# Kernel optimization log

Measured on AMD Instinct MI355X. Metric: run time of the kernel, lower is better.

The kernel has to match this reference:

```python
import jax, jax.numpy as jnp
import numpy as np

# ---- config constants (match init_kwargs / MjModel camera params) ----
PAD_RES = (255, 255)          # padded sensor resolution (Mx, My), odd
RES = (160, 160)              # eye resolution (target_width, target_height)
APERTURE = 0.1                # aperture as fraction of sensor half-size
WAVELENGTHS = (6.1e-07, 5.3e-07, 4.7e-07)  # RGB wavelengths [m]
SENSOR_SIZE = (2e-3, 2e-3)    # (sx, sy) from MjModel.cam_sensorsize [m]


def setup_inputs() -> dict:
    key = jax.random.key(0)
    k1, k2 = jax.random.split(key)
    image = jax.random.uniform(k1, (PAD_RES[0], PAD_RES[1], 3), dtype=jnp.float32)
    depth = jax.random.uniform(k2, (PAD_RES[0], PAD_RES[1]), dtype=jnp.float32)
    return {"image": image, "depth": depth}


def _optics_consts():
    """Precompute the grids of MjCambrianOptics._reset_psf."""
    Mx, My = PAD_RES
    sx, sy = SENSOR_SIZE
    dx, dy = sx / Mx, sy / My
    Lx, Ly = dx * Mx, dy * My
    x1 = jnp.linspace(-Lx / 2.0, Lx / 2.0, Mx, dtype=jnp.float32)
    y1 = jnp.linspace(-Ly / 2.0, Ly / 2.0, My, dtype=jnp.float32)
    X1, Y1 = jnp.meshgrid(x1, y1, indexing='ij')
    fx = jnp.linspace(-1.0 / (2.0 * dx), 1.0 / (2.0 * dx), Mx, dtype=jnp.float32)
    fy = jnp.linspace(-1.0 / (2.0 * dx), 1.0 / (2.0 * dx), My, dtype=jnp.float32)  # dx for both, faithful to source
    FX, FY = jnp.meshgrid(fx, fy, indexing='ij')
    aperture_radius = min(Lx / 2, Ly / 2) * APERTURE + 1e-07
    A = (jnp.sqrt(X1**2 + Y1**2) / aperture_radius <= 1.0).astype(jnp.float32)
    wl = jnp.asarray(WAVELENGTHS, dtype=jnp.float32)[:, None, None]  # (3,1,1)
    X1_Y1 = X1**2 + Y1**2                                           # (Mx,My)
    H_valid = (jnp.sqrt(FX**2 + FY**2) < 1.0 / wl).astype(jnp.float32)  # (3,Mx,My)
    arg = 1.0 - (wl * FX) ** 2 - (wl * FY) ** 2
    # Source computes sqrt(arg) (NaN where arg<0) then nan_to_num after exp;
    # H_valid is exactly 0 where arg<=0, so clamping arg to 0 yields the same H.
    FX_FY = jnp.sqrt(jnp.maximum(arg, 0.0))                         # (3,Mx,My)
    k = (1j * 2.0 * jnp.pi / wl).astype(jnp.complex64)              # (3,1,1)
    return A, X1_Y1, H_valid, FX_FY, k


def _depth_invariant_psf(mean_depth):
    A, X1_Y1, H_valid, FX_FY, k = _optics_consts()
    # spherical wave from point source at mean_depth, masked by aperture
    u1 = jnp.exp(k * jnp.sqrt(X1_Y1 + mean_depth**2))   # (3,Mx,My) complex64
    u2 = u1 * A
    # angular-spectrum transfer function
    H = H_valid * jnp.exp(k * mean_depth * FX_FY)
    u3 = jnp.fft.ifft2(jnp.fft.fft2(H) * jnp.fft.fft2(u2))
    psf = u3 * u3                                        # complex square, faithful to torch.square
    psf = psf / (jnp.sum(psf) + 1e-07)                   # complex normalization, faithful
    return jnp.real(psf)                                 # (3,Mx,My) float32


def reference(image, depth):
    psf = _depth_invariant_psf(jnp.mean(depth))          # (3,Mx,My)
    img = jnp.transpose(image, (2, 0, 1))[None]          # (1,3,H,W)
    kern = psf[:, None].astype(img.dtype)                # (3,1,Mx,My)
    out = jax.lax.conv_general_dilated(
        img, kern, window_strides=(1, 1), padding='SAME',
        feature_group_count=3, dimension_numbers=('NCHW', 'OIHW', 'NCHW'))
    out = jnp.transpose(out[0], (1, 2, 0))               # (H,W,3)
    width, height = out.shape[0], out.shape[1]
    target_width, target_height = RES
    top = (height - target_height) // 2
    left = (width - target_width) // 2
    out = out[top:top + target_height, left:left + target_width]
    return jnp.clip(out, 0.0, 1.0)
```

## Files before the change

kernel.cpp:

```cpp
#include <hip/hip_runtime.h>
#include <hip/hip_bf16.h>
#include <math.h>


constexpr int M   = 255;
constexpr int NP  = M * M;
constexpr int RESO = 160;

constexpr int IMG_ROWS = 416, IMG_COLS = 448;
constexpr int IMG_CH   = IMG_ROWS * IMG_COLS;
constexpr int IMG_SIDE = 3 * IMG_CH;
constexpr int P4_DI   = 304 * 8;
constexpr int P4_CH   = 256 * P4_DI;
constexpr int P4_SIDE = 3 * P4_CH;

typedef __attribute__((ext_vector_type(8))) short short8;
typedef __attribute__((ext_vector_type(4))) float f32x4;

__device__ __forceinline__ unsigned short f2bf(float f) {
    unsigned int u = __float_as_uint(f);
    unsigned int r = (u + 0x7fffu + ((u >> 16) & 1u)) >> 16;
    return (unsigned short)r;
}
__device__ __forceinline__ float bf2f(unsigned short h) {
    return __uint_as_float(((unsigned int)h) << 16);
}

constexpr int MAXN = 1100;
struct PWForest {
    int kind[MAXN];
    int off[MAXN], len[MAXN];
    int li[MAXN], ri[MAXN];
    int lvl[MAXN];
    int nNode, nLeaf, maxLvl;
    int roots[16], nRoots;
};
constexpr int pwf_build(PWForest& T, int o, int n) {
    if (n <= 128) {
        int id = T.nNode++;
        T.kind[id] = 0; T.off[id] = o; T.len[id] = n;
        T.lvl[id] = 0; T.nLeaf++;
        return id;
    }
    int n2 = (n / 2) - ((n / 2) % 8);
    int a = pwf_build(T, o, n2);
    int b = pwf_build(T, o + n2, n - n2);
    int id = T.nNode++;
    T.kind[id] = 1; T.li[id] = a; T.ri[id] = b;
    int l = (T.lvl[a] > T.lvl[b] ? T.lvl[a] : T.lvl[b]) + 1;
    T.lvl[id] = l; if (l > T.maxLvl) T.maxLvl = l;
    return id;
}
constexpr PWForest pwf_make() {
    PWForest T{};
    int pos = 1, rem = NP - 1;
    while (rem > 0) {
        int c = rem > 8192 ? 8192 : rem;
        T.roots[T.nRoots++] = pwf_build(T, pos, c);
        pos += c; rem -= c;
    }
    return T;
}
constexpr PWForest PW = pwf_make();
static_assert(PW.nNode <= MAXN, "forest overflow");
static_assert(PW.nRoots == 8, "chunk count");

__global__ void k_mleaf(const float* __restrict__ depth, float* __restrict__ val) {
    int id = blockIdx.x * 256 + threadIdx.x;
    if (id >= PW.nNode || PW.kind[id] != 0) return;
    const float* a = depth + PW.off[id];
    int n = PW.len[id];
    float r0 = a[0], r1 = a[1], r2 = a[2], r3 = a[3];
    float r4 = a[4], r5 = a[5], r6 = a[6], r7 = a[7];
    int lim = n - (n % 8);
    int i = 8;
    for (; i < lim; i += 8) {
        r0 += a[i + 0]; r1 += a[i + 1]; r2 += a[i + 2]; r3 += a[i + 3];
        r4 += a[i + 4]; r5 += a[i + 5]; r6 += a[i + 6]; r7 += a[i + 7];
    }
    float res = ((r0 + r1) + (r2 + r3)) + ((r4 + r5) + (r6 + r7));
    for (; i < n; ++i) res += a[i];
    val[id] = res;
}

__global__ void k_mtree(const float* __restrict__ depth, float* __restrict__ val,
                        float* __restrict__ meanp) {
    int tid = threadIdx.x;
    for (int l = 1; l <= PW.maxLvl; ++l) {
        for (int id = tid; id < PW.nNode; id += 256)
            if (PW.kind[id] == 1 && PW.lvl[id] == l)
                val[id] = val[PW.li[id]] + val[PW.ri[id]];
        __syncthreads();
    }
    if (tid == 0) {
        float io1 = depth[0];
        for (int r = 0; r < PW.nRoots; ++r)
            io1 = io1 + val[PW.roots[r]];
        meanp[0] = io1 / 65025.0f;
    }
}

__global__ void k_prep(const float* __restrict__ img, unsigned short* __restrict__ IMG2,
                       float2* __restrict__ W,
                       float2* __restrict__ U2, float2* __restrict__ Hb,
                       const float* __restrict__ meanp,
                       double xstart, double xstep, double xstop,
                       double fstart, double fstep, double fstop,
                       float ap_f) {
#pragma clang fp contract(off)
    int idx = blockIdx.x * 256 + threadIdx.x;
    if (idx < 3 * NP) {
        int c = idx / NP, ij = idx % NP, i = ij / M, j = ij % M;
        const float wls[3] = {6.1e-07f, 5.3e-07f, 4.7e-07f};
        float wl = wls[c];
        float ki = ((float)6.283185307179586) / wl;
        float d  = meanp[0];
        float d2 = d * d;

        float x  = (i == 254) ? (float)xstop : (float)((double)i * xstep + xstart);
        float y  = (j == 254) ? (float)xstop : (float)((double)j * xstep + xstart);
        float fx = (i == 254) ? (float)fstop : (float)((double)i * fstep + fstart);
        float fy = (j == 254) ? (float)fstop : (float)((double)j * fstep + fstart);

        float xx = x * x, yy = y * y;
        float X1Y1 = xx + yy;

        float s  = sqrtf(X1Y1 + d2);
        float th = ki * s;
        float A  = (sqrtf(X1Y1) / ap_f <= 1.0f) ? 1.0f : 0.0f;
        float2 u2v;
        if (A != 0.0f) u2v = make_float2((float)cos((double)th), (float)sin((double)th));
        else           u2v = make_float2(0.0f, 0.0f);

        float a = wl * fx, b = wl * fy;
        float arg = (1.0f - a * a) - b * b;
        float FXY = sqrtf(fmaxf(arg, 0.0f));
        float Hv  = (sqrtf(fx * fx + fy * fy) < (1.0f / wl)) ? 1.0f : 0.0f;
        float kd  = ki * d;
        float ph  = kd * FXY;
        float cph = (float)cos((double)ph), sph = (float)sin((double)ph);
        float2 hv = make_float2(Hv * cph, Hv * sph);

        U2[idx] = u2v;
        Hb[idx] = hv;
        return;
    }
    if (idx < 4 * NP) {
        int e = idx - 3 * NP;
        int n = e / M, k = e % M;
        int m = (n * k) % M;
        double ang = -2.0 * 3.14159265358979323846 * (double)m / 255.0;
        W[e] = make_float2((float)cos(ang), (float)sin(ang));
        return;
    }
    int e = idx - 4 * NP;
    if (e >= IMG_SIDE) return;
    int ch = e / IMG_CH, rem = e % IMG_CH;
    int prow = rem / IMG_COLS, pcol = rem % IMG_COLS;
    int a = prow - 80, b = pcol - 80;
    float v = 0.0f;
    if (a >= 0 && a < M && b >= 0 && b < M) v = img[(a * M + b) * 3 + ch];
    unsigned short hi = f2bf(v);
    unsigned short lo = f2bf(v - bf2f(hi));
    IMG2[e] = hi;
    IMG2[IMG_SIDE + e] = lo;
}

#define CG_LOAD(KT, VA0, WB0, VA1, WB1) { \
    int k0_ = (KT) * 16; \
    { int idx_ = threadIdx.x; \
      int r_ = idx_ >> 4, cc_ = idx_ & 15; \
      int gi_ = i0 + r_, gk_ = k0_ + cc_; \
      VA0 = (gi_ < M && gk_ < M) ? Ab[gi_ * M + gk_] : make_float2(0.f, 0.f); \
      if (conjA) VA0.y = -VA0.y; \
      int r2_ = idx_ >> 5, c2_ = idx_ & 31; \
      int gk2_ = k0_ + r2_, gj_ = j0 + c2_; \
      WB0 = make_float2(0.f, 0.f); \
      if (gk2_ < M && gj_ < M) { \
          WB0 = Bb[gk2_ * M + gj_]; \
          if (B2b) { float2 z_ = B2b[gk2_ * M + gj_]; \
              WB0 = make_float2(WB0.x * z_.x - WB0.y * z_.y, WB0.x * z_.y + WB0.y * z_.x); } \
      } \
      if (conjB) WB0.y = -WB0.y; } \
    { int idx_ = threadIdx.x + 256; \
      int r_ = idx_ >> 4, cc_ = idx_ & 15; \
      int gi_ = i0 + r_, gk_ = k0_ + cc_; \
      VA1 = (gi_ < M && gk_ < M) ? Ab[gi_ * M + gk_] : make_float2(0.f, 0.f); \
      if (conjA) VA1.y = -VA1.y; \
      int r2_ = idx_ >> 5, c2_ = idx_ & 31; \
      int gk2_ = k0_ + r2_, gj_ = j0 + c2_; \
      WB1 = make_float2(0.f, 0.f); \
      if (gk2_ < M && gj_ < M) { \
          WB1 = Bb[gk2_ * M + gj_]; \
          if (B2b) { float2 z_ = B2b[gk2_ * M + gj_]; \
              WB1 = make_float2(WB1.x * z_.x - WB1.y * z_.y, WB1.x * z_.y + WB1.y * z_.x); } \
      } \
      if (conjB) WB1.y = -WB1.y; } }

__global__ __launch_bounds__(256)
void k_cgemm(const float2* __restrict__ A, int aBatch,
             const float2* __restrict__ B, const float2* __restrict__ B2,
             int bBatch, float2* __restrict__ C,
             int conjA, int conjB, float scale) {
    __shared__ float2 As[32][17];
    __shared__ float2 Bs[16][33];
    int c = blockIdx.z;
    int tx = threadIdx.x & 15, ty = threadIdx.x >> 4;
    int i0 = blockIdx.y * 32, j0 = blockIdx.x * 32;
    const float2* Ab = A + (size_t)c * aBatch;
    const float2* Bb = B + (size_t)c * bBatch;
    const float2* B2b = B2 ? (B2 + (size_t)c * bBatch) : nullptr;
    float2 a00 = {0,0}, a01 = {0,0}, a10 = {0,0}, a11 = {0,0};

    int wr0 = threadIdx.x >> 4,  wc0 = threadIdx.x & 15;
    int wr0b = threadIdx.x >> 5, wc0b = threadIdx.x & 31;
    int wr1 = (threadIdx.x + 256) >> 4,  wc1 = (threadIdx.x + 256) & 15;
    int wr1b = (threadIdx.x + 256) >> 5, wc1b = (threadIdx.x + 256) & 31;

    float2 vA0, wB0, vA1, wB1;
    float2 nA0, nB0, nA1, nB1;
    CG_LOAD(0, vA0, wB0, vA1, wB1)

    for (int kt = 0; kt < 16; ++kt) {
        As[wr0][wc0]   = vA0;  Bs[wr0b][wc0b] = wB0;
        As[wr1][wc1]   = vA1;  Bs[wr1b][wc1b] = wB1;
        if (kt < 15) { CG_LOAD(kt + 1, nA0, nB0, nA1, nB1) }
        __syncthreads();
#pragma unroll
        for (int kk = 0; kk < 16; ++kk) {
            float2 p = As[ty][kk], q = As[ty + 16][kk];
            float2 u = Bs[kk][tx], v = Bs[kk][tx + 16];
            a00.x += p.x * u.x - p.y * u.y;  a00.y += p.x * u.y + p.y * u.x;
            a01.x += p.x * v.x - p.y * v.y;  a01.y += p.x * v.y + p.y * v.x;
            a10.x += q.x * u.x - q.y * u.y;  a10.y += q.x * u.y + q.y * u.x;
            a11.x += q.x * v.x - q.y * v.y;  a11.y += q.x * v.y + q.y * v.x;
        }
        __syncthreads();
        vA0 = nA0; wB0 = nB0; vA1 = nA1; wB1 = nB1;
    }
    float2* Cb = C + (size_t)c * NP;
    int gi0 = i0 + ty, gi1 = i0 + ty + 16;
    int gj0 = j0 + tx, gj1 = j0 + tx + 16;
    if (gi0 < M && gj0 < M) Cb[gi0 * M + gj0] = make_float2(a00.x * scale, a00.y * scale);
    if (gi0 < M && gj1 < M) Cb[gi0 * M + gj1] = make_float2(a01.x * scale, a01.y * scale);
    if (gi1 < M && gj0 < M) Cb[gi1 * M + gj0] = make_float2(a10.x * scale, a10.y * scale);
    if (gi1 < M && gj1 < M) Cb[gi1 * M + gj1] = make_float2(a11.x * scale, a11.y * scale);
}

__global__ void k_sred(const float2* __restrict__ U3, double2* __restrict__ spart) {
    __shared__ double sx[256], sy[256];
    int t = threadIdx.x;
    double ax = 0.0, ay = 0.0;
    for (int i = blockIdx.x * 256 + t; i < 3 * NP; i += 64 * 256) {
        double zx = (double)U3[i].x, zy = (double)U3[i].y;
        ax += zx * zx - zy * zy;
        ay += 2.0 * zx * zy;
    }
    sx[t] = ax; sy[t] = ay;
    __syncthreads();
    for (int w = 128; w > 0; w >>= 1) {
        if (t < w) { sx[t] += sx[t + w]; sy[t] += sy[t + w]; }
        __syncthreads();
    }
    if (t == 0) spart[blockIdx.x] = make_double2(sx[0], sy[0]);
}

__global__ void k_sfin(const double2* __restrict__ spart, double* __restrict__ sfin) {
    if (threadIdx.x != 0 || blockIdx.x != 0) return;
    double rx = 0.0, ry = 0.0;
    for (int i = 0; i < 64; ++i) { rx += spart[i].x; ry += spart[i].y; }
    double dsx = rx + 1e-7, dsy = ry;
    sfin[0] = dsx;
    sfin[1] = dsy;
    sfin[2] = 1.0 / (dsx * dsx + dsy * dsy);
}

__global__ void k_p4(const float2* __restrict__ U3, const double* __restrict__ sfin,
                     unsigned short* __restrict__ P4) {
    int idx = blockIdx.x * 256 + threadIdx.x;
    if (idx >= P4_SIDE) return;
    double dsx = sfin[0], dsy = sfin[1], inv = sfin[2];
    int ch = idx / P4_CH, rem = idx % P4_CH;
    int di = rem / P4_DI, rem2 = rem % P4_DI;
    int u = rem2 / 8, t = rem2 % 8;
    int p = u - 16 + t;
    float v = 0.0f;
    if (di < M && p >= 0 && p < M) {
        float2 zf = U3[(ch * M + di) * M + p];
        double zx = (double)zf.x, zy = (double)zf.y;
        double zr = zx * zx - zy * zy;
        double zi = 2.0 * zx * zy;
        v = (float)((zr * dsx + zi * dsy) * inv);
    }
    unsigned short hi = f2bf(v);
    unsigned short lo = f2bf(v - bf2f(hi));
    P4[idx] = hi;
    P4[P4_SIDE + idx] = lo;
}

constexpr int LDS_STRIDE = 312;

#define SB __builtin_amdgcn_sched_barrier(0);

#define REP9(OP) OP(0) OP(1) OP(2) OP(3) OP(4) OP(5) OP(6) OP(7) OP(8)

#define DECLA(i) short8 Ah_##i, Al_##i;
#define DECLB(i) short8 Bh_##i, Bl_##i;

#define LDA(i) Ah_##i = *(const short8*)(prH + 256 * i); \
               Al_##i = *(const short8*)(prL + 256 * i);
#define LDB(i) Bh_##i = *(const short8*)(prH + 256 * i); \
               Bl_##i = *(const short8*)(prL + 256 * i);
#define LOADA(dl) { const unsigned short* prH = pHc + (size_t)(d0 + (dl)) * P4_DI + aoff; \
                    const unsigned short* prL = pLc + (size_t)(d0 + (dl)) * P4_DI + aoff; \
                    REP9(LDA) }
#define LOADB(dl) { const unsigned short* prH = pHc + (size_t)(d0 + (dl)) * P4_DI + aoff; \
                    const unsigned short* prL = pLc + (size_t)(d0 + (dl)) * P4_DI + aoff; \
                    REP9(LDB) }

#define CMA(i) { \
    short8 bh0 = *(const short8*)&ldsI[0][rrow][32 * i + 8 * q]; \
    short8 bl0 = *(const short8*)&ldsI[1][rrow][32 * i + 8 * q]; \
    short8 bh1 = *(const short8*)&ldsI[0][rrow][32 * i + 8 * q + 16]; \
    short8 bl1 = *(const short8*)&ldsI[1][rrow][32 * i + 8 * q + 16]; \
    aHH0 = __builtin_amdgcn_mfma_f32_16x16x32_bf16(Ah_##i, bh0, aHH0, 0, 0, 0); \
    aHL0 = __builtin_amdgcn_mfma_f32_16x16x32_bf16(Ah_##i, bl0, aHL0, 0, 0, 0); \
    aLH0 = __builtin_amdgcn_mfma_f32_16x16x32_bf16(Al_##i, bh0, aLH0, 0, 0, 0); \
    aHH1 = __builtin_amdgcn_mfma_f32_16x16x32_bf16(Ah_##i, bh1, aHH1, 0, 0, 0); \
    aHL1 = __builtin_amdgcn_mfma_f32_16x16x32_bf16(Ah_##i, bl1, aHL1, 0, 0, 0); \
    aLH1 = __builtin_amdgcn_mfma_f32_16x16x32_bf16(Al_##i, bh1, aLH1, 0, 0, 0); }
#define CMB(i) { \
    short8 bh0 = *(const short8*)&ldsI[0][rrow][32 * i + 8 * q]; \
    short8 bl0 = *(const short8*)&ldsI[1][rrow][32 * i + 8 * q]; \
    short8 bh1 = *(const short8*)&ldsI[0][rrow][32 * i + 8 * q + 16]; \
    short8 bl1 = *(const short8*)&ldsI[1][rrow][32 * i + 8 * q + 16]; \
    aHH0 = __builtin_amdgcn_mfma_f32_16x16x32_bf16(Bh_##i, bh0, aHH0, 0, 0, 0); \
    aHL0 = __builtin_amdgcn_mfma_f32_16x16x32_bf16(Bh_##i, bl0, aHL0, 0, 0, 0); \
    aLH0 = __builtin_amdgcn_mfma_f32_16x16x32_bf16(Bl_##i, bh0, aLH0, 0, 0, 0); \
    aHH1 = __builtin_amdgcn_mfma_f32_16x16x32_bf16(Bh_##i, bh1, aHH1, 0, 0, 0); \
    aHL1 = __builtin_amdgcn_mfma_f32_16x16x32_bf16(Bh_##i, bl1, aHL1, 0, 0, 0); \
    aLH1 = __builtin_amdgcn_mfma_f32_16x16x32_bf16(Bl_##i, bh1, aLH1, 0, 0, 0); }
#define COMPA(dl) { int rrow = ln + (dl); REP9(CMA) }
#define COMPB(dl) { int rrow = ln + (dl); REP9(CMB) }

__global__ __launch_bounds__(256, 2)
void k_conv(const unsigned short* __restrict__ IMG2,
            const unsigned short* __restrict__ P4,
            float* __restrict__ PART) {
    __shared__ __align__(16) unsigned short ldsI[2][31][LDS_STRIDE];

    int tid  = threadIdx.x;
    int w    = tid >> 6;
    int lane = tid & 63;
    int ln   = lane & 15;
    int q    = lane >> 4;
    int j0 = blockIdx.x * 32;
    int i0 = blockIdx.y * 16;
    int bz = blockIdx.z;
    int ch = bz >> 4, chunk = bz & 15;
    int d0 = chunk << 4;

    const unsigned short* imgH = IMG2 + ch * IMG_CH;
    const unsigned short* imgL = imgH + IMG_SIDE;
    const unsigned short* pHc  = P4 + ch * P4_CH;
    const unsigned short* pLc  = pHc + P4_SIDE;

    int su0  = 16 + 8 * q - ln;
    int aoff = su0 * 8;

    f32x4 aHH0 = {0.f,0.f,0.f,0.f}, aHL0 = {0.f,0.f,0.f,0.f}, aLH0 = {0.f,0.f,0.f,0.f};
    f32x4 aHH1 = {0.f,0.f,0.f,0.f}, aHL1 = {0.f,0.f,0.f,0.f}, aLH1 = {0.f,0.f,0.f,0.f};

    REP9(DECLA)
    REP9(DECLB)

    int dbase = 4 * w;
    LOADA(dbase + 0)

    int row0 = i0 + d0;
    for (int idx = tid; idx < 2 * 31 * 38; idx += 256) {
        int plane = idx / (31 * 38);
        int rem = idx - plane * (31 * 38);
        int r = rem / 38, c = rem - r * 38;
        const unsigned short* src =
            (plane ? imgL : imgH) + (size_t)(row0 + r) * IMG_COLS + j0 + c * 8;
        *(short8*)&ldsI[plane][r][c * 8] = *(const short8*)src;
    }
    __syncthreads();

    LOADB(dbase + 1)
    SB
    COMPA(dbase + 0)
    SB
    LOADA(dbase + 2)
    SB
    COMPB(dbase + 1)
    SB
    LOADB(dbase + 3)
    SB
    COMPA(dbase + 2)
    SB
    COMPB(dbase + 3)

    f32x4 tot0, tot1;
#pragma unroll
    for (int r = 0; r < 4; ++r) {
        tot0[r] = aHH0[r] + aHL0[r] + aLH0[r];
        tot1[r] = aHH1[r] + aHL1[r] + aLH1[r];
    }

    __syncthreads();
    float* red = (float*)&ldsI[0][0][0];
    if (w) {
#pragma unroll
        for (int r = 0; r < 4; ++r) {
            red[((w - 1) * 64 + lane) * 8 + r]     = tot0[r];
            red[((w - 1) * 64 + lane) * 8 + 4 + r] = tot1[r];
        }
    }
    __syncthreads();
    if (w == 0) {
#pragma unroll
        for (int wv = 0; wv < 3; ++wv)
#pragma unroll
            for (int r = 0; r < 4; ++r) {
                tot0[r] += red[(wv * 64 + lane) * 8 + r];
                tot1[r] += red[(wv * 64 + lane) * 8 + 4 + r];
            }
        float* op = PART + (size_t)bz * (RESO * RESO) + (i0 + ln) * RESO + j0 + 4 * q;
        float4 o0; o0.x = tot0[0]; o0.y = tot0[1]; o0.z = tot0[2]; o0.w = tot0[3];
        float4 o1; o1.x = tot1[0]; o1.y = tot1[1]; o1.z = tot1[2]; o1.w = tot1[3];
        *(float4*)op = o0;
        *(float4*)(op + 16) = o1;
    }
}

__global__ void k_out(const float* __restrict__ PART, float* __restrict__ out) {
    int idx = blockIdx.x * 256 + threadIdx.x;
    if (idx >= 3 * RESO * RESO) return;
    int c = idx / (RESO * RESO), ij = idx % (RESO * RESO);
    float s = 0.0f;
    for (int kz = 0; kz < 16; ++kz)
        s += PART[(size_t)(c * 16 + kz) * (RESO * RESO) + ij];
    s = fminf(fmaxf(s, 0.0f), 1.0f);
    int i = ij / RESO, j = ij % RESO;
    out[(i * RESO + j) * 3 + c] = s;
}

extern "C" void kernel_launch(void* const* d_in, const int* in_sizes, int n_in,
                              void* d_out, int out_size, void* d_ws, size_t ws_size,
                              hipStream_t stream) {
    const float* image = (const float*)d_in[0];
    const float* depth = (const float*)d_in[1];
    float* out = (float*)d_out;

    char* p = (char*)d_ws;
    auto alloc = [&](size_t bytes) { void* r = (void*)p; p += (bytes + 255) & ~(size_t)255; return r; };
    float*   meanp = (float*)alloc(4);
    float*   mval  = (float*)alloc(MAXN * 4);
    double*  sfin  = (double*)alloc(3 * 8);
    float2*  Wf    = (float2*)alloc((size_t)NP * 8);
    float2*  UH    = (float2*)alloc((size_t)6 * NP * 8);
    float2*  Td    = (float2*)alloc((size_t)6 * NP * 8);
    float2*  EF    = (float2*)alloc((size_t)6 * NP * 8);
    float2*  U3    = (float2*)alloc((size_t)3 * NP * 8);
    double2* spart = (double2*)alloc(64 * 16);
    unsigned short* P4   = (unsigned short*)alloc((size_t)2 * P4_SIDE * 2);
    unsigned short* IMG2 = (unsigned short*)alloc((size_t)2 * IMG_SIDE * 2);
    float*   PART  = (float*)alloc((size_t)48 * RESO * RESO * 4);

    float2* U2 = UH;
    float2* Hb = UH + (size_t)3 * NP;

    double dx = 0.002 / 255.0;
    double Lx = dx * 255.0;
    double ap = (Lx / 2.0) * 0.1 + 1e-7;
    float ap_f = (float)ap;

    double xstart = -(Lx / 2.0);
    double xstop  =  Lx / 2.0;
    double xstep  = (xstop - xstart) / 254.0;
    double fstart = -1.0 / (2.0 * dx);
    double fstop  =  1.0 / (2.0 * dx);
    double fstep  = (fstop - fstart) / 254.0;

    k_mleaf<<<(PW.nNode + 255) / 256, 256, 0, stream>>>(depth, mval);
    k_mtree<<<1, 256, 0, stream>>>(depth, mval, meanp);
    int gprep = (4 * NP + IMG_SIDE + 255) / 256;
    k_prep<<<gprep, 256, 0, stream>>>(image, IMG2, Wf, U2, Hb, meanp,
                                      xstart, xstep, xstop,
                                      fstart, fstep, fstop, ap_f);

    dim3 bb(256);
    k_cgemm<<<dim3(8, 8, 6), bb, 0, stream>>>(Wf, 0, UH, nullptr, NP, Td, 0, 0, 1.0f);
    k_cgemm<<<dim3(8, 8, 6), bb, 0, stream>>>(Td, NP, Wf, nullptr, 0, EF, 0, 0, 1.0f);
    k_cgemm<<<dim3(8, 8, 3), bb, 0, stream>>>(Wf, 0, EF + (size_t)3 * NP, EF, NP,
                                              Td, 1, 0, 1.0f / 255.0f);
    k_cgemm<<<dim3(8, 8, 3), bb, 0, stream>>>(Td, NP, Wf, nullptr, 0, U3, 0, 1,
                                              1.0f / 255.0f);

    k_sred<<<64, 256, 0, stream>>>(U3, spart);
    k_sfin<<<1, 64, 0, stream>>>(spart, sfin);
    k_p4<<<(P4_SIDE + 255) / 256, 256, 0, stream>>>(U3, sfin, P4);

    k_conv<<<dim3(5, 10, 48), 256, 0, stream>>>(IMG2, P4, PART);
    k_out<<<300, 256, 0, stream>>>(PART, out);
}
```

Measured before the change: 271.2 us.

## Halve cgemm tile rows for more blocks and XOR-swizzle conv LDS image tile

The complex GEMM kernels used for the DFT now use 128-thread blocks computing 16x32 output tiles, which doubles the grid so more of the GPU's compute units get work on these small 255x255 problems. Each thread now loads four B elements per k-step, so B-tile global traffic per output rises. Separately, the convolution kernel's LDS image tile is XOR-swizzled by row (stride padded to 320) to cut bank conflicts on the short8 MFMA operand reads. The swizzle must match between the store and the load paths, and the wider stride uses a bit more shared memory.

```diff
diff --git a/kernel.cpp b/kernel.cpp
--- a/kernel.cpp
+++ b/kernel.cpp
@@ -166,13 +166,19 @@
     IMG2[IMG_SIDE + e] = lo;
 }
 
-#define CG_LOAD(KT, VA0, WB0, VA1, WB1) { \
+#define CG_LOAD(KT, VA0, VA1, WB0, WB1, WB2, WB3) { \
     int k0_ = (KT) * 16; \
     { int idx_ = threadIdx.x; \
       int r_ = idx_ >> 4, cc_ = idx_ & 15; \
       int gi_ = i0 + r_, gk_ = k0_ + cc_; \
       VA0 = (gi_ < M && gk_ < M) ? Ab[gi_ * M + gk_] : make_float2(0.f, 0.f); \
-      if (conjA) VA0.y = -VA0.y; \
+      if (conjA) VA0.y = -VA0.y; } \
+    { int idx_ = threadIdx.x + 128; \
+      int r_ = idx_ >> 4, cc_ = idx_ & 15; \
+      int gi_ = i0 + r_, gk_ = k0_ + cc_; \
+      VA1 = (gi_ < M && gk_ < M) ? Ab[gi_ * M + gk_] : make_float2(0.f, 0.f); \
+      if (conjA) VA1.y = -VA1.y; } \
+    { int idx_ = threadIdx.x; \
       int r2_ = idx_ >> 5, c2_ = idx_ & 31; \
       int gk2_ = k0_ + r2_, gj_ = j0 + c2_; \
       WB0 = make_float2(0.f, 0.f); \
@@ -182,11 +188,7 @@
               WB0 = make_float2(WB0.x * z_.x - WB0.y * z_.y, WB0.x * z_.y + WB0.y * z_.x); } \
       } \
       if (conjB) WB0.y = -WB0.y; } \
-    { int idx_ = threadIdx.x + 256; \
-      int r_ = idx_ >> 4, cc_ = idx_ & 15; \
-      int gi_ = i0 + r_, gk_ = k0_ + cc_; \
-      VA1 = (gi_ < M && gk_ < M) ? Ab[gi_ * M + gk_] : make_float2(0.f, 0.f); \
-      if (conjA) VA1.y = -VA1.y; \
+    { int idx_ = threadIdx.x + 128; \
       int r2_ = idx_ >> 5, c2_ = idx_ & 31; \
       int gk2_ = k0_ + r2_, gj_ = j0 + c2_; \
       WB1 = make_float2(0.f, 0.f); \
@@ -195,40 +197,63 @@
           if (B2b) { float2 z_ = B2b[gk2_ * M + gj_]; \
               WB1 = make_float2(WB1.x * z_.x - WB1.y * z_.y, WB1.x * z_.y + WB1.y * z_.x); } \
       } \
-      if (conjB) WB1.y = -WB1.y; } }
-
-__global__ __launch_bounds__(256)
+      if (conjB) WB1.y = -WB1.y; } \
+    { int idx_ = threadIdx.x + 256; \
+      int r2_ = idx_ >> 5, c2_ = idx_ & 31; \
+      int gk2_ = k0_ + r2_, gj_ = j0 + c2_; \
+      WB2 = make_float2(0.f, 0.f); \
+      if (gk2_ < M && gj_ < M) { \
+          WB2 = Bb[gk2_ * M + gj_]; \
+          if (B2b) { float2 z_ = B2b[gk2_ * M + gj_]; \
+              WB2 = make_float2(WB2.x * z_.x - WB2.y * z_.y, WB2.x * z_.y + WB2.y * z_.x); } \
+      } \
+      if (conjB) WB2.y = -WB2.y; } \
+    { int idx_ = threadIdx.x + 384; \
+      int r2_ = idx_ >> 5, c2_ = idx_ & 31; \
+      int gk2_ = k0_ + r2_, gj_ = j0 + c2_; \
+      WB3 = make_float2(0.f, 0.f); \
+      if (gk2_ < M && gj_ < M) { \
+          WB3 = Bb[gk2_ * M + gj_]; \
+          if (B2b) { float2 z_ = B2b[gk2_ * M + gj_]; \
+              WB3 = make_float2(WB3.x * z_.x - WB3.y * z_.y, WB3.x * z_.y + WB3.y * z_.x); } \
+      } \
+      if (conjB) WB3.y = -WB3.y; } }
+
+__global__ __launch_bounds__(128)
 void k_cgemm(const float2* __restrict__ A, int aBatch,
              const float2* __restrict__ B, const float2* __restrict__ B2,
              int bBatch, float2* __restrict__ C,
              int conjA, int conjB, float scale) {
-    __shared__ float2 As[32][17];
+    __shared__ float2 As[16][17];
     __shared__ float2 Bs[16][33];
     int c = blockIdx.z;
-    int tx = threadIdx.x & 15, ty = threadIdx.x >> 4;
-    int i0 = blockIdx.y * 32, j0 = blockIdx.x * 32;
+    int tx = threadIdx.x & 15, ty = (threadIdx.x >> 4) & 7;
+    int i0 = blockIdx.y * 16, j0 = blockIdx.x * 32;
     const float2* Ab = A + (size_t)c * aBatch;
     const float2* Bb = B + (size_t)c * bBatch;
     const float2* B2b = B2 ? (B2 + (size_t)c * bBatch) : nullptr;
     float2 a00 = {0,0}, a01 = {0,0}, a10 = {0,0}, a11 = {0,0};
 
-    int wr0 = threadIdx.x >> 4,  wc0 = threadIdx.x & 15;
-    int wr0b = threadIdx.x >> 5, wc0b = threadIdx.x & 31;
-    int wr1 = (threadIdx.x + 256) >> 4,  wc1 = (threadIdx.x + 256) & 15;
-    int wr1b = (threadIdx.x + 256) >> 5, wc1b = (threadIdx.x + 256) & 31;
-
-    float2 vA0, wB0, vA1, wB1;
-    float2 nA0, nB0, nA1, nB1;
-    CG_LOAD(0, vA0, wB0, vA1, wB1)
+    int wrA0 = threadIdx.x >> 4,          wcA0 = threadIdx.x & 15;
+    int wrA1 = (threadIdx.x + 128) >> 4,  wcA1 = (threadIdx.x + 128) & 15;
+    int wrB0 = threadIdx.x >> 5,          wcB0 = threadIdx.x & 31;
+    int wrB1 = (threadIdx.x + 128) >> 5,  wcB1 = (threadIdx.x + 128) & 31;
+    int wrB2 = (threadIdx.x + 256) >> 5,  wcB2 = (threadIdx.x + 256) & 31;
+    int wrB3 = (threadIdx.x + 384) >> 5,  wcB3 = (threadIdx.x + 384) & 31;
+
+    float2 vA0, vA1, wB0, wB1, wB2, wB3;
+    float2 nA0, nA1, nB0, nB1, nB2, nB3;
+    CG_LOAD(0, vA0, vA1, wB0, wB1, wB2, wB3)
 
     for (int kt = 0; kt < 16; ++kt) {
-        As[wr0][wc0]   = vA0;  Bs[wr0b][wc0b] = wB0;
-        As[wr1][wc1]   = vA1;  Bs[wr1b][wc1b] = wB1;
-        if (kt < 15) { CG_LOAD(kt + 1, nA0, nB0, nA1, nB1) }
+        As[wrA0][wcA0] = vA0;  As[wrA1][wcA1] = vA1;
+        Bs[wrB0][wcB0] = wB0;  Bs[wrB1][wcB1] = wB1;
+        Bs[wrB2][wcB2] = wB2;  Bs[wrB3][wcB3] = wB3;
+        if (kt < 15) { CG_LOAD(kt + 1, nA0, nA1, nB0, nB1, nB2, nB3) }
         __syncthreads();
 #pragma unroll
         for (int kk = 0; kk < 16; ++kk) {
-            float2 p = As[ty][kk], q = As[ty + 16][kk];
+            float2 p = As[ty][kk], q = As[ty + 8][kk];
             float2 u = Bs[kk][tx], v = Bs[kk][tx + 16];
             a00.x += p.x * u.x - p.y * u.y;  a00.y += p.x * u.y + p.y * u.x;
             a01.x += p.x * v.x - p.y * v.y;  a01.y += p.x * v.y + p.y * v.x;
@@ -236,10 +261,10 @@
             a11.x += q.x * v.x - q.y * v.y;  a11.y += q.x * v.y + q.y * v.x;
         }
         __syncthreads();
-        vA0 = nA0; wB0 = nB0; vA1 = nA1; wB1 = nB1;
+        vA0 = nA0; vA1 = nA1; wB0 = nB0; wB1 = nB1; wB2 = nB2; wB3 = nB3;
     }
     float2* Cb = C + (size_t)c * NP;
-    int gi0 = i0 + ty, gi1 = i0 + ty + 16;
+    int gi0 = i0 + ty, gi1 = i0 + ty + 8;
     int gj0 = j0 + tx, gj1 = j0 + tx + 16;
     if (gi0 < M && gj0 < M) Cb[gi0 * M + gj0] = make_float2(a00.x * scale, a00.y * scale);
     if (gi0 < M && gj1 < M) Cb[gi0 * M + gj1] = make_float2(a01.x * scale, a01.y * scale);
@@ -298,7 +323,7 @@
     P4[P4_SIDE + idx] = lo;
 }
 
-constexpr int LDS_STRIDE = 312;
+constexpr int LDS_STRIDE = 320;
 
 #define SB __builtin_amdgcn_sched_barrier(0);
 
@@ -319,10 +344,10 @@
                     REP9(LDB) }
 
 #define CMA(i) { \
-    short8 bh0 = *(const short8*)&ldsI[0][rrow][32 * i + 8 * q]; \
-    short8 bl0 = *(const short8*)&ldsI[1][rrow][32 * i + 8 * q]; \
-    short8 bh1 = *(const short8*)&ldsI[0][rrow][32 * i + 8 * q + 16]; \
-    short8 bl1 = *(const short8*)&ldsI[1][rrow][32 * i + 8 * q + 16]; \
+    short8 bh0 = *(const short8*)&ldsI[0][rrow][(32 * i + 8 * q) ^ sw]; \
+    short8 bl0 = *(const short8*)&ldsI[1][rrow][(32 * i + 8 * q) ^ sw]; \
+    short8 bh1 = *(const short8*)&ldsI[0][rrow][(32 * i + 8 * q + 16) ^ sw]; \
+    short8 bl1 = *(const short8*)&ldsI[1][rrow][(32 * i + 8 * q + 16) ^ sw]; \
     aHH0 = __builtin_amdgcn_mfma_f32_16x16x32_bf16(Ah_##i, bh0, aHH0, 0, 0, 0); \
     aHL0 = __builtin_amdgcn_mfma_f32_16x16x32_bf16(Ah_##i, bl0, aHL0, 0, 0, 0); \
     aLH0 = __builtin_amdgcn_mfma_f32_16x16x32_bf16(Al_##i, bh0, aLH0, 0, 0, 0); \
@@ -330,18 +355,18 @@
     aHL1 = __builtin_amdgcn_mfma_f32_16x16x32_bf16(Ah_##i, bl1, aHL1, 0, 0, 0); \
     aLH1 = __builtin_amdgcn_mfma_f32_16x16x32_bf16(Al_##i, bh1, aLH1, 0, 0, 0); }
 #define CMB(i) { \
-    short8 bh0 = *(const short8*)&ldsI[0][rrow][32 * i + 8 * q]; \
-    short8 bl0 = *(const short8*)&ldsI[1][rrow][32 * i + 8 * q]; \
-    short8 bh1 = *(const short8*)&ldsI[0][rrow][32 * i + 8 * q + 16]; \
-    short8 bl1 = *(const short8*)&ldsI[1][rrow][32 * i + 8 * q + 16]; \
+    short8 bh0 = *(const short8*)&ldsI[0][rrow][(32 * i + 8 * q) ^ sw]; \
+    short8 bl0 = *(const short8*)&ldsI[1][rrow][(32 * i + 8 * q) ^ sw]; \
+    short8 bh1 = *(const short8*)&ldsI[0][rrow][(32 * i + 8 * q + 16) ^ sw]; \
+    short8 bl1 = *(const short8*)&ldsI[1][rrow][(32 * i + 8 * q + 16) ^ sw]; \
     aHH0 = __builtin_amdgcn_mfma_f32_16x16x32_bf16(Bh_##i, bh0, aHH0, 0, 0, 0); \
     aHL0 = __builtin_amdgcn_mfma_f32_16x16x32_bf16(Bh_##i, bl0, aHL0, 0, 0, 0); \
     aLH0 = __builtin_amdgcn_mfma_f32_16x16x32_bf16(Bl_##i, bh0, aLH0, 0, 0, 0); \
     aHH1 = __builtin_amdgcn_mfma_f32_16x16x32_bf16(Bh_##i, bh1, aHH1, 0, 0, 0); \
     aHL1 = __builtin_amdgcn_mfma_f32_16x16x32_bf16(Bh_##i, bl1, aHL1, 0, 0, 0); \
     aLH1 = __builtin_amdgcn_mfma_f32_16x16x32_bf16(Bl_##i, bh1, aLH1, 0, 0, 0); }
-#define COMPA(dl) { int rrow = ln + (dl); REP9(CMA) }
-#define COMPB(dl) { int rrow = ln + (dl); REP9(CMB) }
+#define COMPA(dl) { int rrow = ln + (dl); int sw = (rrow & 7) << 3; REP9(CMA) }
+#define COMPB(dl) { int rrow = ln + (dl); int sw = (rrow & 7) << 3; REP9(CMB) }
 
 __global__ __launch_bounds__(256, 2)
 void k_conv(const unsigned short* __restrict__ IMG2,
@@ -384,7 +409,7 @@
         int r = rem / 38, c = rem - r * 38;
         const unsigned short* src =
             (plane ? imgL : imgH) + (size_t)(row0 + r) * IMG_COLS + j0 + c * 8;
-        *(short8*)&ldsI[plane][r][c * 8] = *(const short8*)src;
+        *(short8*)&ldsI[plane][r][(c ^ (r & 7)) * 8] = *(const short8*)src;
     }
     __syncthreads();
 
@@ -491,13 +516,13 @@
                                       xstart, xstep, xstop,
                                       fstart, fstep, fstop, ap_f);
 
-    dim3 bb(256);
-    k_cgemm<<<dim3(8, 8, 6), bb, 0, stream>>>(Wf, 0, UH, nullptr, NP, Td, 0, 0, 1.0f);
-    k_cgemm<<<dim3(8, 8, 6), bb, 0, stream>>>(Td, NP, Wf, nullptr, 0, EF, 0, 0, 1.0f);
-    k_cgemm<<<dim3(8, 8, 3), bb, 0, stream>>>(Wf, 0, EF + (size_t)3 * NP, EF, NP,
-                                              Td, 1, 0, 1.0f / 255.0f);
-    k_cgemm<<<dim3(8, 8, 3), bb, 0, stream>>>(Td, NP, Wf, nullptr, 0, U3, 0, 1,
-                                              1.0f / 255.0f);
+    dim3 bb(128);
+    k_cgemm<<<dim3(8, 16, 6), bb, 0, stream>>>(Wf, 0, UH, nullptr, NP, Td, 0, 0, 1.0f);
+    k_cgemm<<<dim3(8, 16, 6), bb, 0, stream>>>(Td, NP, Wf, nullptr, 0, EF, 0, 0, 1.0f);
+    k_cgemm<<<dim3(8, 16, 3), bb, 0, stream>>>(Wf, 0, EF + (size_t)3 * NP, EF, NP,
+                                               Td, 1, 0, 1.0f / 255.0f);
+    k_cgemm<<<dim3(8, 16, 3), bb, 0, stream>>>(Td, NP, Wf, nullptr, 0, U3, 0, 1,
+                                               1.0f / 255.0f);
 
     k_sred<<<64, 256, 0, stream>>>(U3, spart);
     k_sfin<<<1, 64, 0, stream>>>(spart, sfin);
```

New measurement: 289.0 us. +6.6%, slower.
